# Kernel tuning notes

Measured on AMD Instinct MI355X. Metric: run time of the kernel, lower is better.

Reference implementation:

```python
import jax, jax.numpy as jnp
import numpy as np

N = 100_000          # nodes
E = 1_600_000        # random edges (self-loops added inside gat_conv, as PyG does)
F_IN = 14
DIM = 8
HEADS = 8
NEG_SLOPE = 0.2      # PyG GATConv default negative_slope


def _gat_conv(x, edge_index, W, a_src, a_dst, bias, heads, dim, concat):
    """Faithful PyG GATConv (eval mode): self-loops, per-head linear,
    leaky-relu attention logits, segment softmax over dst, scatter-add."""
    n = x.shape[0]
    loop = jnp.arange(n)
    src = jnp.concatenate([edge_index[0], loop])   # source j
    dst = jnp.concatenate([edge_index[1], loop])   # target i (aggregation index)

    h = (x @ W).reshape(n, heads, dim)             # [N, H, D]
    alpha_src = jnp.einsum('nhd,hd->nh', h, a_src)  # [N, H]
    alpha_dst = jnp.einsum('nhd,hd->nh', h, a_dst)

    e = jax.nn.leaky_relu(alpha_src[src] + alpha_dst[dst], NEG_SLOPE)  # [E', H]
    # segment softmax over incoming edges of each dst node
    m = jax.ops.segment_max(e, dst, num_segments=n)                     # [N, H]
    ex = jnp.exp(e - m[dst])
    s = jax.ops.segment_sum(ex, dst, num_segments=n)
    alpha = ex / (s[dst] + 1e-16)                                       # [E', H]

    msg = h[src] * alpha[:, :, None]                                    # [E', H, D]
    out = jax.ops.segment_sum(msg, dst, num_segments=n)                 # [N, H, D]
    out = out.reshape(n, heads * dim) if concat else out.mean(axis=1)
    return out + bias


def setup_inputs() -> dict:
    key = jax.random.key(0)
    ks = jax.random.split(key, 10)
    x = jax.random.normal(ks[0], (N, F_IN), jnp.float32)
    edge_index = jax.random.randint(ks[1], (2, E), 0, N, dtype=jnp.int64)
    W1 = jax.random.normal(ks[2], (F_IN, HEADS * DIM), jnp.float32) * 0.3
    att_src1 = jax.random.normal(ks[3], (HEADS, DIM), jnp.float32) * 0.3
    att_dst1 = jax.random.normal(ks[4], (HEADS, DIM), jnp.float32) * 0.3
    bias1 = jnp.zeros((HEADS * DIM,), jnp.float32)
    W2 = jax.random.normal(ks[5], (HEADS * DIM, DIM), jnp.float32) * 0.15
    att_src2 = jax.random.normal(ks[6], (1, DIM), jnp.float32) * 0.3
    att_dst2 = jax.random.normal(ks[7], (1, DIM), jnp.float32) * 0.3
    bias2 = jnp.zeros((DIM,), jnp.float32)
    return {"x": x, "edge_index": edge_index,
            "W1": W1, "att_src1": att_src1, "att_dst1": att_dst1, "bias1": bias1,
            "W2": W2, "att_src2": att_src2, "att_dst2": att_dst2, "bias2": bias2}


def reference(x, edge_index, W1, att_src1, att_dst1, bias1,
              W2, att_src2, att_dst2, bias2):
    # dropout layers are identity in eval mode
    h = jax.nn.elu(_gat_conv(x, edge_index, W1, att_src1, att_dst1, bias1,
                             HEADS, DIM, concat=True))      # [N, 64]
    out = _gat_conv(h, edge_index, W2, att_src2, att_dst2, bias2,
                    1, DIM, concat=False)                   # [N, 8]
    return out
```

## Files before the change

### kernel.cpp

```cpp
#include <hip/hip_runtime.h>
#include <math.h>

#define F_IN 14
#define NSLOPE 0.2f
#define BSHIFT 7
#define BSZ 128
#define CAP 4096
#define NBMAX 1024
#define NCHUNKMAX 256
#define CHUNK 8192

typedef __attribute__((ext_vector_type(8))) unsigned short u16x8;

__device__ __forceinline__ float leaky(float v) { return v >= 0.f ? v : NSLOPE * v; }

__device__ __forceinline__ float b2f(unsigned short u) {
    union { float f; unsigned int i; } v; v.i = ((unsigned int)u) << 16; return v.f;
}
__device__ __forceinline__ unsigned short f2b(float f) {
    union { float f; unsigned int i; } v; v.f = f;
    unsigned int r = v.i + 0x7FFFu + ((v.i >> 16) & 1u);
    return (unsigned short)(r >> 16);
}

__device__ __forceinline__ int wave_incl_scan(int x) {
#pragma unroll
    for (int off = 1; off < 64; off <<= 1) {
        int v = __shfl_up(x, off, 64);
        if ((threadIdx.x & 63) >= off) x += v;
    }
    return x;
}


__global__ __launch_bounds__(1024)
void k_scatter_k1(const int* __restrict__ ei, int E,
                  int* __restrict__ stage, int* __restrict__ tab, int NB,
                  int nchunk,
                  const float* __restrict__ x,
                  const float* __restrict__ W1,
                  const float* __restrict__ a_src,
                  const float* __restrict__ a_dst,
                  unsigned short* __restrict__ h1b,
                  unsigned short* __restrict__ as1b,
                  unsigned short* __restrict__ ad1b,
                  int N)
{
    __shared__ int hist[NBMAX];
    __shared__ int cur[NBMAX];
    __shared__ int srt[CHUNK];
    __shared__ int wsum[16];
    __shared__ float W[F_IN * 64];
    int t = threadIdx.x;
    if (blockIdx.x < (unsigned)nchunk) {
        int base = blockIdx.x * CHUNK;
        int end = min(base + CHUNK, E);
        int cnt = end - base;
        hist[t] = 0;
        __syncthreads();
        for (int k = base + t; k < end; k += 1024)
            atomicAdd(&hist[ei[E + k] >> BSHIFT], 1);
        __syncthreads();
        int hx = hist[t];
        int incl = wave_incl_scan(hx);
        int wid = t >> 6;
        if ((t & 63) == 63) wsum[wid] = incl;
        __syncthreads();
        int wpre = 0;
#pragma unroll
        for (int w = 0; w < 15; ++w) wpre += (w < wid) ? wsum[w] : 0;
        int exb = incl - hx + wpre;
        cur[t] = exb;
        if (t < NB) tab[(size_t)blockIdx.x * (NBMAX + 1) + t] = exb;
        if (t == 0) tab[(size_t)blockIdx.x * (NBMAX + 1) + NB] = cnt;
        __syncthreads();
        for (int k = base + t; k < end; k += 1024) {
            int j = ei[k];
            int i = ei[E + k];
            int key = i >> BSHIFT;
            int pos = atomicAdd(&cur[key], 1);
            srt[pos] = j | ((i & (BSZ - 1)) << 17);
        }
        __syncthreads();
        int cnt4 = cnt & ~3;
        for (int k = t * 4; k < cnt4; k += 4096) {
            int4 v = *(const int4*)&srt[k];
            *(int4*)&stage[base + k] = v;
        }
        if (t < (cnt & 3)) stage[base + cnt4 + t] = srt[cnt4 + t];
    } else {
        for (int idx = t; idx < F_IN * 64; idx += 1024) W[idx] = W1[idx];
        __syncthreads();
        int node = (blockIdx.x - nchunk) * 16 + (t >> 6);
        int f = t & 63;
        if (node >= N) return;
        const float* xr = x + (size_t)node * F_IN;
        float h = 0.f;
#pragma unroll
        for (int k = 0; k < F_IN; ++k) h += xr[k] * W[k * 64 + f];
        int head = f >> 3, d = f & 7;
        float vs = h * a_src[f];
        float vd = h * a_dst[f];
        vs += __shfl_xor(vs, 1, 8); vs += __shfl_xor(vs, 2, 8); vs += __shfl_xor(vs, 4, 8);
        vd += __shfl_xor(vd, 1, 8); vd += __shfl_xor(vd, 2, 8); vd += __shfl_xor(vd, 4, 8);
        if (d == 0) {
            as1b[node * 8 + head] = f2b(vs);
            ad1b[node * 8 + head] = f2b(vd);
        }
        h1b[(size_t)node * 64 + f] = f2b(h);
    }
}


__global__ __launch_bounds__(256)
void pass2(const int* __restrict__ stage, const int* __restrict__ tab, int nchunk,
           int* __restrict__ rowstart, int* __restrict__ deg,
           int* __restrict__ csr, int N) {
    int b = blockIdx.x;
    int node0 = b << BSHIFT;
    int nn = min(BSZ, N - node0);
    int base = b * CAP;
    __shared__ int segstart[NCHUNKMAX];
    __shared__ int cum[NCHUNKMAX];
    __shared__ int hist[BSZ];
    __shared__ int cur[BSZ];
    __shared__ int wsum[4];
    __shared__ int wsum2[2];
    __shared__ int recs[CAP];
    int t = threadIdx.x;
    int len = 0, s = 0;
    if (t < nchunk) {
        const int* tr = tab + (size_t)t * (NBMAX + 1);
        s = tr[b];
        len = tr[b + 1] - s;
    }
    segstart[t] = s;
    if (t < BSZ) hist[t] = 0;
    int incl = wave_incl_scan(len);
    int wid = t >> 6;
    if ((t & 63) == 63) wsum[wid] = incl;
    __syncthreads();
    int wpre = 0;
#pragma unroll
    for (int w = 0; w < 3; ++w) wpre += (w < wid) ? wsum[w] : 0;
    cum[t] = incl + wpre;
    __syncthreads();
    int cnt = min(cum[NCHUNKMAX - 1], CAP);
    for (int k = t; k < cnt; k += 256) {
        int lo = 0, hi = NCHUNKMAX - 1;
        while (lo < hi) {
            int mid = (lo + hi) >> 1;
            if (cum[mid] > k) hi = mid; else lo = mid + 1;
        }
        int prev = lo ? cum[lo - 1] : 0;
        int r = stage[lo * CHUNK + segstart[lo] + (k - prev)];
        recs[k] = r;
        atomicAdd(&hist[r >> 17], 1);
    }
    __syncthreads();
    int hx = (t < BSZ) ? hist[t] : 0;
    int incl2 = wave_incl_scan(hx);
    if (t < BSZ && (t & 63) == 63) wsum2[t >> 6] = incl2;
    __syncthreads();
    if (t < nn) {
        int ex = incl2 - hx + ((t >= 64) ? wsum2[0] : 0);
        rowstart[node0 + t] = base + ex;
        deg[node0 + t] = hist[t];
        cur[t] = base + ex;
    }
    __syncthreads();
    for (int k = t; k < cnt; k += 256) {
        int r = recs[k];
        int pos = atomicAdd(&cur[r >> 17], 1);
        csr[pos] = r & 0x1FFFF;
    }
}


__global__ void k2_fused(const int* __restrict__ rowstart,
                         const int* __restrict__ deg,
                         const int* __restrict__ csr,
                         const unsigned short* __restrict__ h1b,
                         const unsigned short* __restrict__ as1b,
                         const unsigned short* __restrict__ ad1b,
                         const float* __restrict__ bias1,
                         const float* __restrict__ W2,
                         float* __restrict__ h2, int N)
{
    int t = threadIdx.x;
    int node = blockIdx.x * 32 + (t >> 3);
    int head = t & 7;
    if (node >= N) return;
    float adi = b2f(ad1b[node * 8 + head]);
    float asi = b2f(as1b[node * 8 + head]);
    float ex = __expf(leaky(asi + adi));
    float den = ex;
    u16x8 a = *(const u16x8*)(h1b + (size_t)node * 64 + head * 8);
    float n[8];
#pragma unroll
    for (int u = 0; u < 8; ++u) n[u] = ex * b2f(a[u]);
    int base = rowstart[node], cnt = deg[node];
    int k = 0;
    for (; k + 4 <= cnt; k += 4) {
        int j0 = csr[base + k];
        int j1 = csr[base + k + 1];
        int j2 = csr[base + k + 2];
        int j3 = csr[base + k + 3];
        float e0 = __expf(leaky(b2f(as1b[j0 * 8 + head]) + adi));
        float e1 = __expf(leaky(b2f(as1b[j1 * 8 + head]) + adi));
        float e2 = __expf(leaky(b2f(as1b[j2 * 8 + head]) + adi));
        float e3 = __expf(leaky(b2f(as1b[j3 * 8 + head]) + adi));
        u16x8 r0 = *(const u16x8*)(h1b + (size_t)j0 * 64 + head * 8);
        u16x8 r1 = *(const u16x8*)(h1b + (size_t)j1 * 64 + head * 8);
        u16x8 r2 = *(const u16x8*)(h1b + (size_t)j2 * 64 + head * 8);
        u16x8 r3 = *(const u16x8*)(h1b + (size_t)j3 * 64 + head * 8);
        den += (e0 + e1) + (e2 + e3);
#pragma unroll
        for (int u = 0; u < 8; ++u)
            n[u] += (e0 * b2f(r0[u]) + e1 * b2f(r1[u])) + (e2 * b2f(r2[u]) + e3 * b2f(r3[u]));
    }
    for (; k < cnt; ++k) {
        int j0 = csr[base + k];
        float e0 = __expf(leaky(b2f(as1b[j0 * 8 + head]) + adi));
        u16x8 r0 = *(const u16x8*)(h1b + (size_t)j0 * 64 + head * 8);
        den += e0;
#pragma unroll
        for (int u = 0; u < 8; ++u) n[u] += e0 * b2f(r0[u]);
    }
    float inv = 1.f / (den + 1e-16f);
    float v[8];
    const float* bp = bias1 + head * 8;
#pragma unroll
    for (int u = 0; u < 8; ++u) {
        float w = n[u] * inv + bp[u];
        v[u] = w > 0.f ? w : (__expf(w) - 1.f);
    }
    float p[8];
    const float* wrow = W2 + head * 64;
#pragma unroll
    for (int o = 0; o < 8; ++o) {
        float s = 0.f;
#pragma unroll
        for (int u = 0; u < 8; ++u) s += v[u] * wrow[u * 8 + o];
        p[o] = s;
    }
#pragma unroll
    for (int o = 0; o < 8; ++o) {
        p[o] += __shfl_xor(p[o], 1, 8);
        p[o] += __shfl_xor(p[o], 2, 8);
        p[o] += __shfl_xor(p[o], 4, 8);
    }
    float hv = p[0];
#pragma unroll
    for (int o = 1; o < 8; ++o) hv = (head == o) ? p[o] : hv;
    h2[(size_t)node * 8 + head] = hv;
}


__global__ void k4_gather_l2(const int* __restrict__ rowstart,
                             const int* __restrict__ deg,
                             const int* __restrict__ csr,
                             const float* __restrict__ h2,
                             const float* __restrict__ asw2,
                             const float* __restrict__ adw2,
                             const float* __restrict__ bias2,
                             float* __restrict__ out, int N)
{
    int t = threadIdx.x;
    int node = blockIdx.x * 32 + (t >> 3);
    int d = t & 7;
    if (node >= N) return;
    float aswd = asw2[d], adwd = adw2[d];
    float selfv = h2[(size_t)node * 8 + d];
    float td = selfv * adwd;
    td += __shfl_xor(td, 1, 8); td += __shfl_xor(td, 2, 8); td += __shfl_xor(td, 4, 8);
    float adi = td;
    float ts = selfv * aswd;
    ts += __shfl_xor(ts, 1, 8); ts += __shfl_xor(ts, 2, 8); ts += __shfl_xor(ts, 4, 8);
    float ex = __expf(leaky(ts + adi));
    float den = ex;
    float num = ex * selfv;
    int base = rowstart[node], cnt = deg[node];
    int k = 0;
    for (; k + 4 <= cnt; k += 4) {
        int j0 = csr[base + k];
        int j1 = csr[base + k + 1];
        int j2 = csr[base + k + 2];
        int j3 = csr[base + k + 3];
        float v0 = h2[(size_t)j0 * 8 + d];
        float v1 = h2[(size_t)j1 * 8 + d];
        float v2 = h2[(size_t)j2 * 8 + d];
        float v3 = h2[(size_t)j3 * 8 + d];
        float t0 = v0 * aswd, t1 = v1 * aswd, t2 = v2 * aswd, t3 = v3 * aswd;
        t0 += __shfl_xor(t0, 1, 8); t1 += __shfl_xor(t1, 1, 8);
        t2 += __shfl_xor(t2, 1, 8); t3 += __shfl_xor(t3, 1, 8);
        t0 += __shfl_xor(t0, 2, 8); t1 += __shfl_xor(t1, 2, 8);
        t2 += __shfl_xor(t2, 2, 8); t3 += __shfl_xor(t3, 2, 8);
        t0 += __shfl_xor(t0, 4, 8); t1 += __shfl_xor(t1, 4, 8);
        t2 += __shfl_xor(t2, 4, 8); t3 += __shfl_xor(t3, 4, 8);
        float e0 = __expf(leaky(t0 + adi));
        float e1 = __expf(leaky(t1 + adi));
        float e2 = __expf(leaky(t2 + adi));
        float e3 = __expf(leaky(t3 + adi));
        den += (e0 + e1) + (e2 + e3);
        num += (e0 * v0 + e1 * v1) + (e2 * v2 + e3 * v3);
    }
    for (; k < cnt; ++k) {
        int j0 = csr[base + k];
        float v0 = h2[(size_t)j0 * 8 + d];
        float t0 = v0 * aswd;
        t0 += __shfl_xor(t0, 1, 8); t0 += __shfl_xor(t0, 2, 8); t0 += __shfl_xor(t0, 4, 8);
        float e0 = __expf(leaky(t0 + adi));
        den += e0;
        num += e0 * v0;
    }
    out[(size_t)node * 8 + d] = num / (den + 1e-16f) + bias2[d];
}


extern "C" void kernel_launch(void* const* d_in, const int* in_sizes, int n_in,
                              void* d_out, int out_size, void* d_ws, size_t ws_size,
                              hipStream_t stream) {
    const float* x    = (const float*)d_in[0];
    const int*   ei   = (const int*)d_in[1];
    const float* W1   = (const float*)d_in[2];
    const float* asw1 = (const float*)d_in[3];
    const float* adw1 = (const float*)d_in[4];
    const float* b1   = (const float*)d_in[5];
    const float* W2   = (const float*)d_in[6];
    const float* asw2 = (const float*)d_in[7];
    const float* adw2 = (const float*)d_in[8];
    const float* b2   = (const float*)d_in[9];
    float* out = (float*)d_out;

    int N = in_sizes[0] / F_IN;
    int E = in_sizes[1] / 2;
    int NB = (N + BSZ - 1) >> BSHIFT;
    int nchunk = (E + CHUNK - 1) / CHUNK;
    int k1blk = (N + 15) / 16;

    float* fw  = (float*)d_ws;
    float* h2  = fw;
    unsigned short* h1b  = (unsigned short*)(h2 + (size_t)N * 8);
    unsigned short* as1b = h1b + (size_t)N * 64;
    unsigned short* ad1b = as1b + (size_t)N * 8;
    int* deg      = (int*)(ad1b + (size_t)N * 8);
    int* rowstart = deg + N;
    int* csr      = rowstart + N;
    int* stage    = csr + (size_t)NB * CAP;
    int* tab      = stage + (size_t)nchunk * CHUNK;

    k_scatter_k1<<<nchunk + k1blk, 1024, 0, stream>>>(ei, E, stage, tab, NB, nchunk,
                                                      x, W1, asw1, adw1,
                                                      h1b, as1b, ad1b, N);
    pass2<<<NB, 256, 0, stream>>>(stage, tab, nchunk, rowstart, deg, csr, N);

    k2_fused<<<(N + 31) / 32, 256, 0, stream>>>(rowstart, deg, csr, h1b, as1b, ad1b,
                                                b1, W2, h2, N);

    k4_gather_l2<<<(N + 31) / 32, 256, 0, stream>>>(rowstart, deg, csr, h2,
                                                    asw2, adw2, b2, out, N);
}
```

Baseline: 122.7 us.

## Degree-sort nodes within buckets for layer-1 gather and batch k1 nodes per block

pass2 now counting-sorts the nodes of each 128-node bucket by in-degree (capped at 63) and writes a permutation array. k2_fused walks nodes in that order, so each wavefront holds nodes of similar degree and idles less on divergent loop lengths. Separately, the node-feature part of k_scatter_k1 handles 64 nodes per block in four passes and reads W1 from global memory instead of staging it in shared memory, cutting the block count and the shared memory used by those blocks. The cost is an extra indirection per node in k2, a small amount of added sort work in pass2, and less coalesced h2 writes.

```diff
diff --git a/kernel.cpp b/kernel.cpp
--- a/kernel.cpp
+++ b/kernel.cpp
@@ -50,7 +50,6 @@
     __shared__ int cur[NBMAX];
     __shared__ int srt[CHUNK];
     __shared__ int wsum[16];
-    __shared__ float W[F_IN * 64];
     int t = threadIdx.x;
     if (blockIdx.x < (unsigned)nchunk) {
         int base = blockIdx.x * CHUNK;
@@ -89,25 +88,28 @@
         }
         if (t < (cnt & 3)) stage[base + cnt4 + t] = srt[cnt4 + t];
     } else {
-        for (int idx = t; idx < F_IN * 64; idx += 1024) W[idx] = W1[idx];
-        __syncthreads();
-        int node = (blockIdx.x - nchunk) * 16 + (t >> 6);
         int f = t & 63;
-        if (node >= N) return;
-        const float* xr = x + (size_t)node * F_IN;
-        float h = 0.f;
-#pragma unroll
-        for (int k = 0; k < F_IN; ++k) h += xr[k] * W[k * 64 + f];
-        int head = f >> 3, d = f & 7;
-        float vs = h * a_src[f];
-        float vd = h * a_dst[f];
-        vs += __shfl_xor(vs, 1, 8); vs += __shfl_xor(vs, 2, 8); vs += __shfl_xor(vs, 4, 8);
-        vd += __shfl_xor(vd, 1, 8); vd += __shfl_xor(vd, 2, 8); vd += __shfl_xor(vd, 4, 8);
-        if (d == 0) {
-            as1b[node * 8 + head] = f2b(vs);
-            ad1b[node * 8 + head] = f2b(vd);
+        int g = t >> 6;
+        int node0 = (blockIdx.x - nchunk) * 64;
+#pragma unroll
+        for (int pass = 0; pass < 4; ++pass) {
+            int node = node0 + pass * 16 + g;
+            if (node >= N) break;
+            const float* xr = x + (size_t)node * F_IN;
+            float h = 0.f;
+#pragma unroll
+            for (int k = 0; k < F_IN; ++k) h += xr[k] * W1[k * 64 + f];
+            int head = f >> 3, d = f & 7;
+            float vs = h * a_src[f];
+            float vd = h * a_dst[f];
+            vs += __shfl_xor(vs, 1, 8); vs += __shfl_xor(vs, 2, 8); vs += __shfl_xor(vs, 4, 8);
+            vd += __shfl_xor(vd, 1, 8); vd += __shfl_xor(vd, 2, 8); vd += __shfl_xor(vd, 4, 8);
+            if (d == 0) {
+                as1b[node * 8 + head] = f2b(vs);
+                ad1b[node * 8 + head] = f2b(vd);
+            }
+            h1b[(size_t)node * 64 + f] = f2b(h);
         }
-        h1b[(size_t)node * 64 + f] = f2b(h);
     }
 }
 
@@ -115,7 +117,7 @@
 __global__ __launch_bounds__(256)
 void pass2(const int* __restrict__ stage, const int* __restrict__ tab, int nchunk,
            int* __restrict__ rowstart, int* __restrict__ deg,
-           int* __restrict__ csr, int N) {
+           int* __restrict__ csr, int* __restrict__ order, int N) {
     int b = blockIdx.x;
     int node0 = b << BSHIFT;
     int nn = min(BSZ, N - node0);
@@ -126,6 +128,7 @@
     __shared__ int cur[BSZ];
     __shared__ int wsum[4];
     __shared__ int wsum2[2];
+    __shared__ int dcur[64];
     __shared__ int recs[CAP];
     int t = threadIdx.x;
     int len = 0, s = 0;
@@ -136,6 +139,7 @@
     }
     segstart[t] = s;
     if (t < BSZ) hist[t] = 0;
+    if (t >= 128 && t < 192) dcur[t - 128] = 0;
     int incl = wave_incl_scan(len);
     int wid = t >> 6;
     if ((t & 63) == 63) wsum[wid] = incl;
@@ -161,12 +165,28 @@
     int hx = (t < BSZ) ? hist[t] : 0;
     int incl2 = wave_incl_scan(hx);
     if (t < BSZ && (t & 63) == 63) wsum2[t >> 6] = incl2;
+    int myd = 0;
+    if (t < nn) myd = min(hx, 63);
     __syncthreads();
     if (t < nn) {
         int ex = incl2 - hx + ((t >= 64) ? wsum2[0] : 0);
         rowstart[node0 + t] = base + ex;
-        deg[node0 + t] = hist[t];
+        deg[node0 + t] = hx;
         cur[t] = base + ex;
+        atomicAdd(&dcur[myd], 1);
+    }
+    __syncthreads();
+    if (t < 64) {
+        int v = dcur[t];
+        int inc = wave_incl_scan(v);
+        dcur[t] = inc - v;
+    }
+    __syncthreads();
+    if (t < nn) {
+        int pos = atomicAdd(&dcur[myd], 1);
+        order[node0 + pos] = node0 + t;
+    } else if (t < BSZ) {
+        order[node0 + t] = -1;
     }
     __syncthreads();
     for (int k = t; k < cnt; k += 256) {
@@ -177,7 +197,8 @@
 }
 
 
-__global__ void k2_fused(const int* __restrict__ rowstart,
+__global__ void k2_fused(const int* __restrict__ order,
+                         const int* __restrict__ rowstart,
                          const int* __restrict__ deg,
                          const int* __restrict__ csr,
                          const unsigned short* __restrict__ h1b,
@@ -185,12 +206,14 @@
                          const unsigned short* __restrict__ ad1b,
                          const float* __restrict__ bias1,
                          const float* __restrict__ W2,
-                         float* __restrict__ h2, int N)
+                         float* __restrict__ h2, int NS)
 {
     int t = threadIdx.x;
-    int node = blockIdx.x * 32 + (t >> 3);
+    int slot = blockIdx.x * 32 + (t >> 3);
+    if (slot >= NS) return;
+    int node = order[slot];
+    if (node < 0) return;
     int head = t & 7;
-    if (node >= N) return;
     float adi = b2f(ad1b[node * 8 + head]);
     float asi = b2f(as1b[node * 8 + head]);
     float ex = __expf(leaky(asi + adi));
@@ -336,8 +359,9 @@
     int N = in_sizes[0] / F_IN;
     int E = in_sizes[1] / 2;
     int NB = (N + BSZ - 1) >> BSHIFT;
+    int NS = NB << BSHIFT;
     int nchunk = (E + CHUNK - 1) / CHUNK;
-    int k1blk = (N + 15) / 16;
+    int k1blk = (N + 63) / 64;
 
     float* fw  = (float*)d_ws;
     float* h2  = fw;
@@ -346,17 +370,18 @@
     unsigned short* ad1b = as1b + (size_t)N * 8;
     int* deg      = (int*)(ad1b + (size_t)N * 8);
     int* rowstart = deg + N;
-    int* csr      = rowstart + N;
+    int* order    = rowstart + N;
+    int* csr      = order + NS;
     int* stage    = csr + (size_t)NB * CAP;
     int* tab      = stage + (size_t)nchunk * CHUNK;
 
     k_scatter_k1<<<nchunk + k1blk, 1024, 0, stream>>>(ei, E, stage, tab, NB, nchunk,
                                                       x, W1, asw1, adw1,
                                                       h1b, as1b, ad1b, N);
-    pass2<<<NB, 256, 0, stream>>>(stage, tab, nchunk, rowstart, deg, csr, N);
-
-    k2_fused<<<(N + 31) / 32, 256, 0, stream>>>(rowstart, deg, csr, h1b, as1b, ad1b,
-                                                b1, W2, h2, N);
+    pass2<<<NB, 256, 0, stream>>>(stage, tab, nchunk, rowstart, deg, csr, order, N);
+
+    k2_fused<<<(NS + 31) / 32, 256, 0, stream>>>(order, rowstart, deg, csr, h1b, as1b, ad1b,
+                                                 b1, W2, h2, NS);
 
     k4_gather_l2<<<(N + 31) / 32, 256, 0, stream>>>(rowstart, deg, csr, h2,
                                                     asw2, adw2, b2, out, N);
```

Measured after the change: 125.3 us. +2.1%, slower.
